# Performance work log

Measured on AMD Instinct MI355X. Metric: run time of the kernel, lower is better.

## Reference

```python
import jax, jax.numpy as jnp
import numpy as np
from jax import lax

B, H, W, CIN, COUT, LAT = 8, 128, 128, 256, 256, 512


def lrelu(x):
    return jax.nn.leaky_relu(x, 0.2)


def setup_inputs() -> dict:
    key = jax.random.key(0)
    ks = jax.random.split(key, 9)
    inp = {
        "data": jax.random.normal(ks[0], (B, H, W, CIN), jnp.float32),
        "latent": jax.random.normal(ks[1], (B, LAT), jnp.float32),
        "noise": jax.random.normal(ks[2], (B, H, W, COUT), jnp.float32),
        # ScaledDense std_dense: LAT -> CIN, bias init ones
        "std_W": jax.random.normal(ks[3], (LAT, CIN), jnp.float32),
        "std_b": jnp.ones((CIN,), jnp.float32),
        # 3x3 conv weights (HWIO), N(0,1) init; scaled at call time
        "conv_w": jax.random.normal(ks[4], (3, 3, CIN, COUT), jnp.float32),
        "bias": jnp.zeros((1, 1, 1, COUT), jnp.float32),
        "noise_coef": jnp.zeros((1, 1, 1, COUT), jnp.float32),
        # pointwise denses: COUT -> 4*COUT -> COUT
        "D1_W": jax.random.normal(ks[5], (COUT, 4 * COUT), jnp.float32),
        "D1_b": jnp.zeros((4 * COUT,), jnp.float32),
        "D2_W": jax.random.normal(ks[6], (4 * COUT, COUT), jnp.float32),
        "D2_b": jnp.zeros((COUT,), jnp.float32),
    }
    return inp


def reference(data, latent, noise, std_W, std_b, conv_w, bias, noise_coef,
              D1_W, D1_b, D2_W, D2_b):
    lat_dim = latent.shape[-1]
    cin = conv_w.shape[2]
    cout = conv_w.shape[3]
    # equalized-LR scaled dense: style vector s [B, Cin]
    s = latent @ (std_W * np.float32(np.sqrt(2.0 / lat_dim))) + std_b
    # modulate input channels
    x = data * s[:, None, None, :]
    # scaled 3x3 conv, SAME padding
    w = conv_w * np.float32(np.sqrt(2.0 / (cin * 9)))
    y = lax.conv_general_dilated(
        x, w, window_strides=(1, 1), padding="SAME",
        dimension_numbers=("NHWC", "HWIO", "NHWC"))
    # demodulation: d[b,o] = rsqrt(sum_{k,i} (w[k,i,o]*s[b,i])^2 + eps)
    # computed as small matmul on squared quantities (no [B,3,3,Cin,Cout] tensor)
    w2 = jnp.sum(w * w, axis=(0, 1))                      # [Cin, Cout]
    d = lax.rsqrt(jnp.einsum("io,bi->bo", w2, s * s) + 1e-8)  # [B, Cout]
    y = y * d[:, None, None, :] + bias + noise * noise_coef
    y = lrelu(y)
    h = lrelu(y @ (D1_W * np.float32(np.sqrt(2.0 / cout))) + D1_b)
    out = lrelu(h @ (D2_W * np.float32(np.sqrt(2.0 / (4 * cout)))) + D2_b)
    return out
```

## Files before the change

### kernel.cpp

```cpp
#include <hip/hip_runtime.h>

typedef unsigned short ushort_t;
typedef __attribute__((ext_vector_type(8))) short short8;
typedef __attribute__((ext_vector_type(4))) float f32x4;

#define C1 0.0625f
#define C2 0.029462782549439483f
#define C2SQ (2.0f/2304.0f)
#define C3 0.08838834764831845f
#define C4 0.04419417382415922f

__device__ __forceinline__ float bf2f(ushort_t u) {
  union { unsigned int i; float f; } v; v.i = ((unsigned int)u) << 16; return v.f;
}
__device__ __forceinline__ ushort_t f2bf(float f) {
  union { float f; unsigned int i; } v; v.f = f;
  unsigned int r = v.i + 0x7fffu + ((v.i >> 16) & 1u);
  return (ushort_t)(r >> 16);
}
__device__ __forceinline__ void async16(const void* g, void* l) {
  __builtin_amdgcn_global_load_lds(
      (const __attribute__((address_space(1))) unsigned int*)g,
      (__attribute__((address_space(3))) unsigned int*)l, 16, 0, 0);
}
__device__ __forceinline__ float lrelu(float v) { return v > 0.f ? v : 0.2f * v; }

__global__ void k_style(const float* __restrict__ latent, const float* __restrict__ stdW,
                        const float* __restrict__ stdb, float* __restrict__ s) {
  __shared__ float red[256];
  int b = blockIdx.x, ic = blockIdx.y;
  int il = threadIdx.x & 31, lp = threadIdx.x >> 5;
  int i = (ic << 5) + il;
  float acc = 0.f;
  int l0 = lp << 6;
  for (int l = l0; l < l0 + 64; ++l)
    acc += latent[(b << 9) + l] * stdW[(l << 8) + i];
  red[threadIdx.x] = acc;
  __syncthreads();
  if (lp == 0) {
    float v = 0.f;
#pragma unroll
    for (int p = 0; p < 8; ++p) v += red[(p << 5) + il];
    s[(b << 8) + i] = v * C1 + stdb[i];
  }
}

__global__ void k_w2(const float* __restrict__ convw, float* __restrict__ w2) {
  int t = blockIdx.x * 256 + threadIdx.x;
  float acc = 0.f;
#pragma unroll
  for (int tap = 0; tap < 9; ++tap) {
    float w = convw[tap * 65536 + t];
    acc += w * w;
  }
  w2[t] = acc * C2SQ;
}

__global__ void k_demod(const float* __restrict__ w2, const float* __restrict__ s,
                        float* __restrict__ dm) {
  __shared__ float red[256];
  int b = blockIdx.x, oc = blockIdx.y;
  int ol = threadIdx.x & 31, ip = threadIdx.x >> 5;
  int o = (oc << 5) + ol;
  float acc = 0.f;
  int i0 = ip << 5;
  for (int i = i0; i < i0 + 32; ++i) {
    float si = s[(b << 8) + i];
    acc += w2[(i << 8) + o] * si * si;
  }
  red[threadIdx.x] = acc;
  __syncthreads();
  if (ip == 0) {
    float v = 1e-8f;
#pragma unroll
    for (int p = 0; p < 8; ++p) v += red[(p << 5) + ol];
    dm[(b << 8) + o] = rsqrtf(v);
  }
}

__global__ void k_wt(const float* __restrict__ convw, ushort_t* __restrict__ wt) {
  int t = blockIdx.x * 256 + threadIdx.x;
  int o = t / 2304;
  int kk = t - o * 2304;
  int tap = kk >> 8, i = kk & 255;
  wt[t] = f2bf(convw[tap * 65536 + (i << 8) + o] * C2);
}

__global__ void k_w1t(const float* __restrict__ d1w, ushort_t* __restrict__ w1t) {
  int t = blockIdx.x * 256 + threadIdx.x;
  int n = t >> 8, k = t & 255;
  w1t[t] = f2bf(d1w[(k << 10) + n] * C3);
}
__global__ void k_w2t(const float* __restrict__ d2w, ushort_t* __restrict__ w2t) {
  int t = blockIdx.x * 256 + threadIdx.x;
  int o = t >> 10, k = t & 1023;
  w2t[t] = f2bf(d2w[(k << 8) + o] * C4);
}

__global__ void k_pad(const float* __restrict__ data, const float* __restrict__ s,
                      ushort_t* __restrict__ xs) {
  int tid = blockIdx.x * 256 + threadIdx.x;
  int ci8 = tid & 31;
  int p = tid >> 5;
  int xp = p % 130;
  int q = p / 130;
  int yp = q % 130;
  int b = q / 130;
  short8 ov = {0, 0, 0, 0, 0, 0, 0, 0};
  if (yp >= 1 && yp <= 128 && xp >= 1 && xp <= 128) {
    const f32x4* src = (const f32x4*)(data + ((((b << 7) + (yp - 1)) << 7) + (xp - 1)) * 256 + (ci8 << 3));
    const f32x4* sp  = (const f32x4*)(s + (b << 8) + (ci8 << 3));
    f32x4 v0 = src[0], v1 = src[1];
    f32x4 s0 = sp[0],  s1 = sp[1];
#pragma unroll
    for (int j = 0; j < 4; ++j) ov[j]     = (short)f2bf(v0[j] * s0[j]);
#pragma unroll
    for (int j = 0; j < 4; ++j) ov[4 + j] = (short)f2bf(v1[j] * s1[j]);
  }
  *(short8*)(xs + ((size_t)tid << 3)) = ov;
}


#define SWZ_FLAT(flat, row) ((((flat) ^ (row)) & 7) << 3)

__device__ __forceinline__ void stage_a(const ushort_t* ximg, int y0, int h, int kt2,
                                        int t, ushort_t* dst) {
  int tap = kt2 >> 2;
  int ci0 = (kt2 & 3) << 6;
  int ky = (tap >= 6) ? 2 : (tap >= 3 ? 1 : 0);
  int kx = tap - ky * 3;
  const ushort_t* ga = ximg + ((y0 + h + ky) * 130 + kx) * 256 + ci0;
#pragma unroll
  for (int is = 0; is < 2; ++is) {
    int flat = t + (is << 9);
    int row = flat >> 3;
    int cil = SWZ_FLAT(flat, row);
    async16(ga + row * 256 + cil, dst + (flat << 3));
  }
}

__device__ __forceinline__ void stage_b(const ushort_t* wtp, int h, int kt2, int t, ushort_t* dst) {
  const ushort_t* gb = wtp + (kt2 << 6) + (size_t)(h << 7) * 2304;
#pragma unroll
  for (int is = 0; is < 2; ++is) {
    int flat = t + (is << 9);
    int row = flat >> 3;
    int cil = SWZ_FLAT(flat, row);
    async16(gb + (size_t)row * 2304 + cil, dst + (flat << 3));
  }
}

#define LOAD_A(BASE) {                                                        \
  _Pragma("unroll") for (int q = 0; q < 4; ++q) {                             \
    int lr = (wm << 6) + (q << 4) + (lane & 15);                              \
    int bo0 = (lr << 7) + ((lane >> 4) << 4);                                 \
    int sw = (lr & 7) << 4;                                                   \
    af[q][0] = *(const short8*)((BASE) + ((bo0      ) ^ sw));                 \
    af[q][1] = *(const short8*)((BASE) + ((bo0 + 64 ) ^ sw)); } }

#define LOAD_B(BASE, BF) {                                                    \
  _Pragma("unroll") for (int p = 0; p < 2; ++p) {                             \
    int lr = (wn << 5) + (p << 4) + (lane & 15);                              \
    int bo0 = (lr << 7) + ((lane >> 4) << 4);                                 \
    int sw = (lr & 7) << 4;                                                   \
    BF[p][0] = *(const short8*)((BASE) + ((bo0      ) ^ sw));                 \
    BF[p][1] = *(const short8*)((BASE) + ((bo0 + 64 ) ^ sw)); } }

#define MFMA_BLK(MH, NH, BF) {                                                \
  _Pragma("unroll") for (int q = 0; q < 4; ++q)                               \
    _Pragma("unroll") for (int p = 0; p < 2; ++p)                             \
      _Pragma("unroll") for (int ks = 0; ks < 2; ++ks)                        \
        acc[MH][NH][q][p] = __builtin_amdgcn_mfma_f32_16x16x32_bf16(          \
            af[q][ks], BF[p][ks], acc[MH][NH][q][p], 0, 0, 0); }

#define PH_BAR()  __builtin_amdgcn_s_barrier()
#define PH_LGKM() asm volatile("s_waitcnt lgkmcnt(0)" ::: "memory")
#define VM4()     asm volatile("s_waitcnt vmcnt(4)" ::: "memory")
#define PRIO1()   __builtin_amdgcn_s_setprio(1)
#define PRIO0()   __builtin_amdgcn_s_setprio(0)

__global__ __launch_bounds__(512, 2) void k_conv(
    const ushort_t* __restrict__ xs, const ushort_t* __restrict__ wt,
    const float* __restrict__ dmod, const float* __restrict__ bias,
    const float* __restrict__ ncoef, const float* __restrict__ noise,
    ushort_t* __restrict__ y) {
  __shared__ __align__(16) ushort_t lds[2][4][128 * 64];

  int bid0 = blockIdx.x;
  int bid = (bid0 & 7) * 64 + (bid0 >> 3);
  int m0 = bid << 8;
  int b = m0 >> 14;
  int y0 = (m0 & 16383) >> 7;
  const ushort_t* ximg = xs + (size_t)b * (130 * 130 * 256);

  int t = threadIdx.x;
  int lane = t & 63;
  int wid = t >> 6;
  int wm = wid >> 2, wn = wid & 3;

  const f32x4 fz = {0.f, 0.f, 0.f, 0.f};
  f32x4 acc[2][2][4][2];
#pragma unroll
  for (int a0 = 0; a0 < 2; ++a0)
#pragma unroll
    for (int a1 = 0; a1 < 2; ++a1)
#pragma unroll
      for (int a2 = 0; a2 < 4; ++a2)
#pragma unroll
        for (int a3 = 0; a3 < 2; ++a3) acc[a0][a1][a2][a3] = fz;

  short8 af[4][2], bf[2][2], bg[2][2];

  stage_a(ximg, y0, 0, 0, t, &lds[0][0][0]);
  stage_b(wt,        0, 0, t, &lds[0][2][0]);
  stage_b(wt,        1, 0, t, &lds[0][3][0]);
  stage_a(ximg, y0, 1, 0, t, &lds[0][1][0]);

#pragma unroll 1
  for (int kt = 0; kt < 35; ++kt) {
    int cb = kt & 1, nb = cb ^ 1;
    const char* a0b = (const char*)&lds[cb][0][0];
    const char* a1b = (const char*)&lds[cb][1][0];
    const char* b0b = (const char*)&lds[cb][2][0];
    const char* b1b = (const char*)&lds[cb][3][0];
    int kt2 = kt + 1;
    VM4(); PH_BAR();
    LOAD_A(a0b); LOAD_B(b0b, bf);
    stage_a(ximg, y0, 0, kt2, t, &lds[nb][0][0]);
    PH_BAR(); PH_LGKM();
    PRIO1(); MFMA_BLK(0, 0, bf); PRIO0();
    VM4(); PH_BAR();
    LOAD_B(b1b, bg);
    stage_b(wt, 0, kt2, t, &lds[nb][2][0]);
    PH_BAR(); PH_LGKM();
    PRIO1(); MFMA_BLK(0, 1, bg); PRIO0();
    VM4(); PH_BAR();
    LOAD_A(a1b);
    stage_b(wt, 1, kt2, t, &lds[nb][3][0]);
    PH_BAR(); PH_LGKM();
    PRIO1(); MFMA_BLK(1, 1, bg); PRIO0();
    stage_a(ximg, y0, 1, kt2, t, &lds[nb][1][0]);
    PH_BAR();
    PRIO1(); MFMA_BLK(1, 0, bf); PRIO0();
  }
  {
    const char* a0b = (const char*)&lds[1][0][0];
    const char* a1b = (const char*)&lds[1][1][0];
    const char* b0b = (const char*)&lds[1][2][0];
    const char* b1b = (const char*)&lds[1][3][0];
    asm volatile("s_waitcnt vmcnt(4)" ::: "memory"); PH_BAR();
    LOAD_A(a0b); LOAD_B(b0b, bf);
    PH_BAR(); PH_LGKM();
    PRIO1(); MFMA_BLK(0, 0, bf); PRIO0();
    asm volatile("s_waitcnt vmcnt(2)" ::: "memory"); PH_BAR();
    LOAD_B(b1b, bg);
    PH_BAR(); PH_LGKM();
    PRIO1(); MFMA_BLK(0, 1, bg); PRIO0();
    asm volatile("s_waitcnt vmcnt(0)" ::: "memory"); PH_BAR();
    LOAD_A(a1b);
    PH_BAR(); PH_LGKM();
    PRIO1(); MFMA_BLK(1, 1, bg); PRIO0();
    PH_BAR();
    PRIO1(); MFMA_BLK(1, 0, bf); PRIO0();
  }

#pragma unroll
  for (int mh = 0; mh < 2; ++mh)
#pragma unroll
    for (int nh = 0; nh < 2; ++nh)
#pragma unroll
      for (int p = 0; p < 2; ++p) {
        int o = (nh << 7) + (wn << 5) + (p << 4) + (lane & 15);
        float dv = dmod[(b << 8) + o];
        float bv = bias[o];
        float nc = ncoef[o];
#pragma unroll
        for (int q = 0; q < 4; ++q) {
          int mloc = (mh << 7) + (wm << 6) + (q << 4) + ((lane >> 4) << 2);
#pragma unroll
          for (int r = 0; r < 4; ++r) {
            int idx = (m0 + mloc + r) * 256 + o;
            float v = acc[mh][nh][q][p][r] * dv + bv + noise[idx] * nc;
            y[idx] = f2bf(lrelu(v));
          }
        }
      }
}

__global__ __launch_bounds__(256, 2) void k_dense(
    const ushort_t* __restrict__ y, float* __restrict__ out,
    const ushort_t* __restrict__ w1t, const float* __restrict__ b1,
    const ushort_t* __restrict__ w2t, const float* __restrict__ b2) {
  __shared__ __align__(16) ushort_t a1[2][128 * 32];
  __shared__ __align__(16) ushort_t bb[256 * 32];
  __shared__ __align__(16) ushort_t ly[128 * 136];
  int rb = blockIdx.x;
  int t = threadIdx.x, lane = t & 63;
  int wm = (t >> 7) & 1, wn = (t >> 6) & 1;
  int row0 = rb << 7;

  const f32x4 fz = {0.f, 0.f, 0.f, 0.f};
  f32x4 oacc[4][8];
#pragma unroll
  for (int i = 0; i < 4; ++i) {
#pragma unroll
    for (int j = 0; j < 8; ++j) oacc[i][j] = fz;
  }

#pragma unroll 1
  for (int nc = 0; nc < 8; ++nc) {
    f32x4 hacc[4][4];
#pragma unroll
    for (int i = 0; i < 4; ++i) {
#pragma unroll
      for (int j = 0; j < 4; ++j) hacc[i][j] = fz;
    }
#pragma unroll 1
    for (int kp = 0; kp < 4; ++kp) {
#pragma unroll
      for (int h = 0; h < 2; ++h) {
        int k0 = ((kp << 1) + h) << 5;
#pragma unroll
        for (int r = 0; r < 2; ++r) {
          int flat = t + (r << 8);
          int m = flat >> 2, k8 = (flat & 3) << 3;
          async16(y + (row0 + m) * 256 + k0 + k8, &a1[h][flat << 3]);
          async16(w1t + ((nc << 7) + m) * 256 + k0 + k8, &bb[(h << 12) + (flat << 3)]);
        }
      }
      __syncthreads();
#pragma unroll
      for (int h = 0; h < 2; ++h) {
        short8 af[4], bfr[4];
#pragma unroll
        for (int i = 0; i < 4; ++i) {
          af[i]  = *(const short8*)&a1[h][((wm << 6) + (i << 4) + (lane & 15)) * 32 + ((lane >> 4) << 3)];
          bfr[i] = *(const short8*)&bb[(h << 12) + ((wn << 6) + (i << 4) + (lane & 15)) * 32 + ((lane >> 4) << 3)];
        }
#pragma unroll
        for (int i = 0; i < 4; ++i) {
#pragma unroll
          for (int j = 0; j < 4; ++j)
            hacc[i][j] = __builtin_amdgcn_mfma_f32_16x16x32_bf16(af[i], bfr[j], hacc[i][j], 0, 0, 0);
        }
      }
      __syncthreads();
    }
#pragma unroll
    for (int j = 0; j < 4; ++j) {
      int n = (wn << 6) + (j << 4) + (lane & 15);
      float bv = b1[(nc << 7) + n];
#pragma unroll
      for (int i = 0; i < 4; ++i) {
        int mbase = (wm << 6) + (i << 4) + ((lane >> 4) << 2);
#pragma unroll
        for (int r = 0; r < 4; ++r)
          ly[(mbase + r) * 136 + n] = f2bf(lrelu(hacc[i][j][r] + bv));
      }
    }
    __syncthreads();
#pragma unroll 1
    for (int kc2 = 0; kc2 < 4; ++kc2) {
      int kk0 = kc2 << 5;
#pragma unroll
      for (int r = 0; r < 4; ++r) {
        int flat = t + (r << 8);
        int o = flat >> 2, k8 = (flat & 3) << 3;
        async16(w2t + o * 1024 + (nc << 7) + kk0 + k8, &bb[flat << 3]);
      }
      __syncthreads();
      short8 af2[4];
#pragma unroll
      for (int i = 0; i < 4; ++i)
        af2[i] = *(const short8*)&ly[((wm << 6) + (i << 4) + (lane & 15)) * 136 + kk0 + ((lane >> 4) << 3)];
#pragma unroll
      for (int j = 0; j < 8; ++j) {
        short8 bfr2 = *(const short8*)&bb[((wn << 7) + (j << 4) + (lane & 15)) * 32 + ((lane >> 4) << 3)];
#pragma unroll
        for (int i = 0; i < 4; ++i)
          oacc[i][j] = __builtin_amdgcn_mfma_f32_16x16x32_bf16(af2[i], bfr2, oacc[i][j], 0, 0, 0);
      }
      __syncthreads();
    }
  }
#pragma unroll
  for (int j = 0; j < 8; ++j) {
    int o = (wn << 7) + (j << 4) + (lane & 15);
    float bv = b2[o];
#pragma unroll
    for (int i = 0; i < 4; ++i) {
      int mbase = (wm << 6) + (i << 4) + ((lane >> 4) << 2);
#pragma unroll
      for (int r = 0; r < 4; ++r)
        out[(row0 + mbase + r) * 256 + o] = lrelu(oacc[i][j][r] + bv);
    }
  }
}

extern "C" void kernel_launch(void* const* d_in, const int* in_sizes, int n_in,
                              void* d_out, int out_size, void* d_ws, size_t ws_size,
                              hipStream_t stream) {
  const float* data   = (const float*)d_in[0];
  const float* latent = (const float*)d_in[1];
  const float* noise  = (const float*)d_in[2];
  const float* stdW   = (const float*)d_in[3];
  const float* stdb   = (const float*)d_in[4];
  const float* convw  = (const float*)d_in[5];
  const float* bias   = (const float*)d_in[6];
  const float* ncoef  = (const float*)d_in[7];
  const float* D1W    = (const float*)d_in[8];
  const float* D1b    = (const float*)d_in[9];
  const float* D2W    = (const float*)d_in[10];
  const float* D2b    = (const float*)d_in[11];
  float* out = (float*)d_out;

  char* ws = (char*)d_ws;
  float*    s    = (float*)ws;
  float*    dmod = (float*)(ws + 8192);
  float*    w2   = (float*)(ws + 16384);
  ushort_t* wt   = (ushort_t*)(ws + 278528);
  ushort_t* w1t  = (ushort_t*)(ws + 1458176);
  ushort_t* w2t  = (ushort_t*)(ws + 1982464);
  ushort_t* xs   = (ushort_t*)(ws + 2506752);
  ushort_t* yv   = (ushort_t*)(ws + 71729152);

  k_style<<<dim3(8, 8), 256, 0, stream>>>(latent, stdW, stdb, s);
  k_w2<<<256, 256, 0, stream>>>(convw, w2);
  k_demod<<<dim3(8, 8), 256, 0, stream>>>(w2, s, dmod);
  k_wt<<<2304, 256, 0, stream>>>(convw, wt);
  k_w1t<<<1024, 256, 0, stream>>>(D1W, w1t);
  k_w2t<<<1024, 256, 0, stream>>>(D2W, w2t);
  k_pad<<<16900, 256, 0, stream>>>(data, s, xs);
  k_conv<<<512, 512, 0, stream>>>(xs, wt, dmod, bias, ncoef, noise, yv);
  k_dense<<<1024, 256, 0, stream>>>(yv, out, w1t, D1b, w2t, D2b);
}
```

Before: 703.5 us.

## Restructure fused dense kernel: resident Y tile, register-loaded weights, 8 waves

The fused D1/D2 dense kernel now loads the whole 128x256 input tile into LDS once, using an XOR swizzle. Weight fragments for both matmuls are read straight from global memory into registers with software prefetch, instead of being staged through LDS with a barrier per K step. The block grows to 512 threads (8 waves) with a block-index remap, and the hidden tile in LDS is swizzled to avoid bank conflicts. This cuts many barriers and LDS staging round trips, but each wave now issues uncached-looking global weight reads and LDS use goes up.

```diff
diff --git a/kernel.cpp b/kernel.cpp
--- a/kernel.cpp
+++ b/kernel.cpp
@@ -287,112 +287,149 @@
       }
 }
 
-__global__ __launch_bounds__(256, 2) void k_dense(
+__global__ __launch_bounds__(512, 2) void k_dense(
     const ushort_t* __restrict__ y, float* __restrict__ out,
     const ushort_t* __restrict__ w1t, const float* __restrict__ b1,
     const ushort_t* __restrict__ w2t, const float* __restrict__ b2) {
-  __shared__ __align__(16) ushort_t a1[2][128 * 32];
-  __shared__ __align__(16) ushort_t bb[256 * 32];
-  __shared__ __align__(16) ushort_t ly[128 * 136];
-  int rb = blockIdx.x;
+  __shared__ __align__(16) ushort_t ybuf[128 * 256];
+  __shared__ __align__(16) ushort_t ly[128 * 128];
+
+  int bid0 = blockIdx.x;
+  int bid = (bid0 & 7) * 128 + (bid0 >> 3);
+  int row0 = bid << 7;
   int t = threadIdx.x, lane = t & 63;
-  int wm = (t >> 7) & 1, wn = (t >> 6) & 1;
-  int row0 = rb << 7;
+  int wid = t >> 6;
+  int wm = wid >> 2, wn = wid & 3;
+  int l15 = lane & 15, lhi = lane >> 4;
+
+#pragma unroll
+  for (int is = 0; is < 8; ++is) {
+    int flat = t + (is << 9);
+    int row = flat >> 5, c = flat & 31;
+    int cs = c ^ (row & 7);
+    async16(y + (size_t)(row0 + row) * 256 + (cs << 3), (char*)ybuf + ((size_t)flat << 4));
+  }
+
+  int asw = l15 & 7;
+  int arow[4];
+#pragma unroll
+  for (int q = 0; q < 4; ++q) arow[q] = (wm << 6) + (q << 4) + l15;
 
   const f32x4 fz = {0.f, 0.f, 0.f, 0.f};
-  f32x4 oacc[4][8];
-#pragma unroll
-  for (int i = 0; i < 4; ++i) {
-#pragma unroll
-    for (int j = 0; j < 8; ++j) oacc[i][j] = fz;
-  }
+  f32x4 oacc[4][4];
+#pragma unroll
+  for (int q = 0; q < 4; ++q)
+#pragma unroll
+    for (int p = 0; p < 4; ++p) oacc[q][p] = fz;
+
+  asm volatile("s_waitcnt vmcnt(0)" ::: "memory");
+  __syncthreads();
 
 #pragma unroll 1
   for (int nc = 0; nc < 8; ++nc) {
-    f32x4 hacc[4][4];
-#pragma unroll
-    for (int i = 0; i < 4; ++i) {
-#pragma unroll
-      for (int j = 0; j < 4; ++j) hacc[i][j] = fz;
+    f32x4 hacc[4][2];
+#pragma unroll
+    for (int q = 0; q < 4; ++q)
+#pragma unroll
+      for (int p = 0; p < 2; ++p) hacc[q][p] = fz;
+
+    const ushort_t* w1b = w1t + ((size_t)((nc << 7) + (wn << 5) + l15) << 8) + (lhi << 3);
+    short8 b1f[4][2][2];
+#pragma unroll
+    for (int kt = 0; kt < 2; ++kt)
+#pragma unroll
+      for (int p = 0; p < 2; ++p)
+#pragma unroll
+        for (int ks = 0; ks < 2; ++ks)
+          b1f[kt][p][ks] = *(const short8*)(w1b + (p << 12) + (kt << 6) + (ks << 5));
+
+#pragma unroll
+    for (int kt = 0; kt < 4; ++kt) {
+      if (kt < 2) {
+#pragma unroll
+        for (int p = 0; p < 2; ++p)
+#pragma unroll
+          for (int ks = 0; ks < 2; ++ks)
+            b1f[kt + 2][p][ks] = *(const short8*)(w1b + (p << 12) + ((kt + 2) << 6) + (ks << 5));
+      }
+      short8 af[4][2];
+#pragma unroll
+      for (int q = 0; q < 4; ++q)
+#pragma unroll
+        for (int ks = 0; ks < 2; ++ks)
+          af[q][ks] = *(const short8*)((const char*)ybuf +
+              (arow[q] << 9) + (kt << 7) + ((((ks << 2) + lhi) ^ asw) << 4));
+#pragma unroll
+      for (int q = 0; q < 4; ++q)
+#pragma unroll
+        for (int p = 0; p < 2; ++p)
+#pragma unroll
+          for (int ks = 0; ks < 2; ++ks)
+            hacc[q][p] = __builtin_amdgcn_mfma_f32_16x16x32_bf16(
+                af[q][ks], b1f[kt][p][ks], hacc[q][p], 0, 0, 0);
     }
-#pragma unroll 1
-    for (int kp = 0; kp < 4; ++kp) {
-#pragma unroll
-      for (int h = 0; h < 2; ++h) {
-        int k0 = ((kp << 1) + h) << 5;
-#pragma unroll
-        for (int r = 0; r < 2; ++r) {
-          int flat = t + (r << 8);
-          int m = flat >> 2, k8 = (flat & 3) << 3;
-          async16(y + (row0 + m) * 256 + k0 + k8, &a1[h][flat << 3]);
-          async16(w1t + ((nc << 7) + m) * 256 + k0 + k8, &bb[(h << 12) + (flat << 3)]);
+
+    __syncthreads();
+
+    const ushort_t* w2b = w2t + ((size_t)((wn << 6) + l15) << 10) + (nc << 7) + (lhi << 3);
+    short8 b2f[4][4];
+#pragma unroll
+    for (int ks = 0; ks < 2; ++ks)
+#pragma unroll
+      for (int p = 0; p < 4; ++p)
+        b2f[ks][p] = *(const short8*)(w2b + (p << 14) + (ks << 5));
+
+    float b1v0 = b1[(nc << 7) + (wn << 5) + l15];
+    float b1v1 = b1[(nc << 7) + (wn << 5) + 16 + l15];
+#pragma unroll
+    for (int q = 0; q < 4; ++q)
+#pragma unroll
+      for (int p = 0; p < 2; ++p) {
+        float bv = p ? b1v1 : b1v0;
+        int nbase = (wn << 5) + (p << 4) + l15;
+        int nch = nbase >> 3;
+        int nlo = (nbase & 7) << 1;
+#pragma unroll
+        for (int r = 0; r < 4; ++r) {
+          int m = (wm << 6) + (q << 4) + (lhi << 2) + r;
+          int byt = (m << 8) + ((nch ^ (m & 7)) << 4) + nlo;
+          *(ushort_t*)((char*)ly + byt) = f2bf(lrelu(hacc[q][p][r] + bv));
         }
       }
-      __syncthreads();
-#pragma unroll
-      for (int h = 0; h < 2; ++h) {
-        short8 af[4], bfr[4];
-#pragma unroll
-        for (int i = 0; i < 4; ++i) {
-          af[i]  = *(const short8*)&a1[h][((wm << 6) + (i << 4) + (lane & 15)) * 32 + ((lane >> 4) << 3)];
-          bfr[i] = *(const short8*)&bb[(h << 12) + ((wn << 6) + (i << 4) + (lane & 15)) * 32 + ((lane >> 4) << 3)];
-        }
-#pragma unroll
-        for (int i = 0; i < 4; ++i) {
-#pragma unroll
-          for (int j = 0; j < 4; ++j)
-            hacc[i][j] = __builtin_amdgcn_mfma_f32_16x16x32_bf16(af[i], bfr[j], hacc[i][j], 0, 0, 0);
-        }
+    __syncthreads();
+
+#pragma unroll
+    for (int ks = 0; ks < 4; ++ks) {
+      if (ks < 2) {
+#pragma unroll
+        for (int p = 0; p < 4; ++p)
+          b2f[ks + 2][p] = *(const short8*)(w2b + (p << 14) + ((ks + 2) << 5));
       }
-      __syncthreads();
+      short8 af2[4];
+#pragma unroll
+      for (int q = 0; q < 4; ++q)
+        af2[q] = *(const short8*)((const char*)ly +
+            (arow[q] << 8) + ((((ks << 2) + lhi) ^ asw) << 4));
+#pragma unroll
+      for (int q = 0; q < 4; ++q)
+#pragma unroll
+        for (int p = 0; p < 4; ++p)
+          oacc[q][p] = __builtin_amdgcn_mfma_f32_16x16x32_bf16(
+              af2[q], b2f[ks][p], oacc[q][p], 0, 0, 0);
     }
-#pragma unroll
-    for (int j = 0; j < 4; ++j) {
-      int n = (wn << 6) + (j << 4) + (lane & 15);
-      float bv = b1[(nc << 7) + n];
-#pragma unroll
-      for (int i = 0; i < 4; ++i) {
-        int mbase = (wm << 6) + (i << 4) + ((lane >> 4) << 2);
-#pragma unroll
-        for (int r = 0; r < 4; ++r)
-          ly[(mbase + r) * 136 + n] = f2bf(lrelu(hacc[i][j][r] + bv));
+  }
+
+#pragma unroll
+  for (int p = 0; p < 4; ++p) {
+    int o = (wn << 6) + (p << 4) + l15;
+    float bv = b2[o];
+#pragma unroll
+    for (int q = 0; q < 4; ++q) {
+#pragma unroll
+      for (int r = 0; r < 4; ++r) {
+        int m = (wm << 6) + (q << 4) + (lhi << 2) + r;
+        out[(size_t)(row0 + m) * 256 + o] = lrelu(oacc[q][p][r] + bv);
       }
-    }
-    __syncthreads();
-#pragma unroll 1
-    for (int kc2 = 0; kc2 < 4; ++kc2) {
-      int kk0 = kc2 << 5;
-#pragma unroll
-      for (int r = 0; r < 4; ++r) {
-        int flat = t + (r << 8);
-        int o = flat >> 2, k8 = (flat & 3) << 3;
-        async16(w2t + o * 1024 + (nc << 7) + kk0 + k8, &bb[flat << 3]);
-      }
-      __syncthreads();
-      short8 af2[4];
-#pragma unroll
-      for (int i = 0; i < 4; ++i)
-        af2[i] = *(const short8*)&ly[((wm << 6) + (i << 4) + (lane & 15)) * 136 + kk0 + ((lane >> 4) << 3)];
-#pragma unroll
-      for (int j = 0; j < 8; ++j) {
-        short8 bfr2 = *(const short8*)&bb[((wn << 7) + (j << 4) + (lane & 15)) * 32 + ((lane >> 4) << 3)];
-#pragma unroll
-        for (int i = 0; i < 4; ++i)
-          oacc[i][j] = __builtin_amdgcn_mfma_f32_16x16x32_bf16(af2[i], bfr2, oacc[i][j], 0, 0, 0);
-      }
-      __syncthreads();
-    }
-  }
-#pragma unroll
-  for (int j = 0; j < 8; ++j) {
-    int o = (wn << 7) + (j << 4) + (lane & 15);
-    float bv = b2[o];
-#pragma unroll
-    for (int i = 0; i < 4; ++i) {
-      int mbase = (wm << 6) + (i << 4) + ((lane >> 4) << 2);
-#pragma unroll
-      for (int r = 0; r < 4; ++r)
-        out[(row0 + mbase + r) * 256 + o] = lrelu(oacc[i][j][r] + bv);
     }
   }
 }
@@ -432,5 +469,5 @@
   k_w2t<<<1024, 256, 0, stream>>>(D2W, w2t);
   k_pad<<<16900, 256, 0, stream>>>(data, s, xs);
   k_conv<<<512, 512, 0, stream>>>(xs, wt, dmod, bias, ncoef, noise, yv);
-  k_dense<<<1024, 256, 0, stream>>>(yv, out, w1t, D1b, w2t, D2b);
-}
+  k_dense<<<1024, 512, 0, stream>>>(yv, out, w1t, D1b, w2t, D2b);
+}
```

Measured after the change: 783.5 us. 1.11x slower.
